# Performance work log

Measured on AMD Instinct MI355X. Metric: run time of the kernel, lower is better.

Reference implementation:

```python
import jax, jax.numpy as jnp
import numpy as np

B, L, H, G, NH, DH, FF = 16, 512, 1024, 2, 16, 64, 4096
DM = H // G          # per-group d_model = 512
LG = L // G          # inner attention seq len = 256
EPS = 1e-6


def _ln(x, g, b):
    m = x.mean(-1, keepdims=True)
    v = ((x - m) ** 2).mean(-1, keepdims=True)
    return (x - m) * jax.lax.rsqrt(v + EPS) * g + b


def setup_inputs() -> dict:
    key = jax.random.key(0)
    ks = jax.random.split(key, 12)
    sd = 0.02
    n = lambda k, sh: jax.random.normal(k, sh, jnp.float32) * sd
    return {
        "y": jax.random.normal(ks[0], (B, L, H), jnp.float32),
        "y_mask": jax.random.randint(ks[1], (B, 1, 1, LG), 0, 2).astype(bool),
        # MHAtt projections (operate on per-group d_model = DM)
        "Wv": n(ks[2], (DM, DM)), "bv": jnp.zeros((DM,), jnp.float32),
        "Wk": n(ks[3], (DM, DM)), "bk": jnp.zeros((DM,), jnp.float32),
        "Wq": n(ks[4], (DM, DM)), "bq": jnp.zeros((DM,), jnp.float32),
        # merge projection (full hidden)
        "Wm": n(ks[5], (H, H)), "bm": jnp.zeros((H,), jnp.float32),
        # GFFN: linear1 H->FF, linear2 grouped FF/G -> H/G
        "W1": n(ks[6], (H, FF)), "b1": jnp.zeros((FF,), jnp.float32),
        "W2": n(ks[7], (FF // G, H // G)), "b2": jnp.zeros((H // G,), jnp.float32),
        # LayerNorms
        "g1": jnp.ones((H,), jnp.float32), "beta1": jnp.zeros((H,), jnp.float32),
        "g2": jnp.ones((H,), jnp.float32), "beta2": jnp.zeros((H,), jnp.float32),
    }


def reference(y, y_mask, Wv, bv, Wk, bk, Wq, bq, Wm, bm, W1, b1, W2, b2,
              g1, beta1, g2, beta2):
    b, l, d = y.shape
    # group reshuffle: split channels into G groups, stack along batch
    yg = jnp.concatenate(jnp.split(y, G, axis=-1), axis=0)        # (b*G, l, DM)
    mask = jnp.tile(y_mask, (G, 1, 1, 1))                          # (b*G, 1, 1, l/G)

    # projections; view uses h*dh = H so inner seq becomes l/G
    q = (yg @ Wq + bq).reshape(b * G, -1, NH, DH).transpose(0, 2, 1, 3)  # (bG, NH, l/G, DH)
    k = (yg @ Wk + bk).reshape(b * G, -1, NH, DH).transpose(0, 2, 1, 3)
    v = (yg @ Wv + bv).reshape(b * G, -1, NH, DH).transpose(0, 2, 1, 3)

    scores = jnp.einsum('bhqd,bhkd->bhqk', q, k) / np.sqrt(DH)
    scores = jnp.where(mask, jnp.float32(-1e9), scores)
    att = jax.nn.softmax(scores, axis=-1)                          # dropout = identity (eval)
    ctx = jnp.einsum('bhqk,bhkd->bhqd', att, v)                    # (bG, NH, l/G, DH)
    ctx = ctx.transpose(0, 2, 1, 3).reshape(b * G, -1, DM)         # (bG, l, DM)

    atted = jnp.concatenate(jnp.split(ctx, G, axis=0), axis=-1)    # (b, l, H)
    atted = atted @ Wm + bm
    y1 = _ln(y + atted, g1, beta1)

    # GFFN
    h1 = jax.nn.relu(y1 @ W1 + b1)                                  # (b, l, FF)
    h2 = jnp.einsum('blgf,fo->blgo', h1.reshape(b, l, G, FF // G), W2) + b2
    ff = h2.reshape(b, l, H)
    return _ln(y1 + ff, g2, beta2)
```

## Files before the change

### kernel.cpp

```cpp
#include <hip/hip_runtime.h>
#include <stdint.h>

typedef unsigned short u16;
using us8   = __attribute__((ext_vector_type(8))) unsigned short;
using us4   = __attribute__((ext_vector_type(4))) unsigned short;
using bf16x8 = __attribute__((ext_vector_type(8))) __bf16;
using f32x4 = __attribute__((ext_vector_type(4))) float;

#define DEV static __device__ __forceinline__

DEV float bf2f(u16 u) { union { uint32_t i; float f; } v; v.i = (uint32_t)u << 16; return v.f; }
DEV u16 f2bf(float f) {
    union { float f; uint32_t i; } v; v.f = f;
    uint32_t u = v.i;
    return (u16)((u + 0x7FFFu + ((u >> 16) & 1u)) >> 16);
}

DEV void async16(const u16* g, u16* ldsbase)
{
    __builtin_amdgcn_global_load_lds((const __attribute__((address_space(1))) void*)g,
                                     (__attribute__((address_space(3))) void*)ldsbase, 16, 0, 0);
}

struct DetectArgs { const void* p[18]; int nw[18]; };

__global__ __launch_bounds__(256) void k_detect_all(DetectArgs a, int* flags)
{
    const int b = blockIdx.x;
    const int t = threadIdx.x;
    __shared__ int cnt[4];
    if (t < 4) cnt[t] = 0;
    __syncthreads();
    if (b == 1) {
        const uint8_t* m = (const uint8_t*)a.p[1];
        int c0 = 0, c1 = 0, c2 = 0, c3 = 0;
        for (int i = t; i < 4096; i += 256) {
            uint8_t v = m[i];
            int mod = i & 3;
            if (v == 0x3F && mod == 1) c0++;
            if (v == 0x3F && mod == 3) c1++;
            if (v == 1 && mod != 0) c2++;
            if (v == 1 && mod == 0) c3++;
        }
        atomicAdd(&cnt[0], c0); atomicAdd(&cnt[1], c1); atomicAdd(&cnt[2], c2); atomicAdd(&cnt[3], c3);
        __syncthreads();
        if (t == 0) {
            int mf;
            if (cnt[0] > 0) mf = 2;
            else if (cnt[1] > 0) mf = 3;
            else if (cnt[2] > 0) mf = 0;
            else if (cnt[3] > 0) mf = 1;
            else mf = 0;
            flags[1] = mf;
        }
    } else {
        const u16* p = (const u16*)a.p[b];
        int nw = a.nw[b];
        int nze = 0, pe = 0, nzo = 0;
        for (int i = t; i < nw; i += 256) {
            u16 w = p[i];
            if (w == 0) continue;
            int e = (w >> 7) & 0xFF;
            bool pl = (e >= 90 && e <= 140);
            if ((i & 1) == 0) { nze++; if (pl) pe++; }
            else nzo++;
        }
        atomicAdd(&cnt[0], nze); atomicAdd(&cnt[1], pe); atomicAdd(&cnt[2], nzo);
        __syncthreads();
        if (t == 0) {
            int f;
            if (cnt[0] > 0)      f = (cnt[1] * 10 >= cnt[0] * 6) ? 2 : 3;
            else if (cnt[2] > 0) f = 3;
            else                 f = 2;
            flags[b] = f;
        }
    }
}

__global__ __launch_bounds__(256) void k_expand_mask(const void* mask, const int* flag, float* mb)
{
    int i = blockIdx.x * 256 + threadIdx.x;
    if (i >= 4096) return;
    int f = *flag;
    bool on;
    if (f == 0)      on = ((const uint8_t*)mask)[i]  != 0;
    else if (f == 1) on = ((const int*)mask)[i]      != 0;
    else if (f == 2) on = ((const u16*)mask)[i]      != 0;
    else             on = ((const uint32_t*)mask)[i] != 0;
    mb[i] = on ? -1e9f : 0.0f;
}

__global__ __launch_bounds__(256) void k_convert_bf(const void* src, u16* dst, int n, const int* flag)
{
    int i = blockIdx.x * 256 + threadIdx.x;
    if (i >= n) return;
    if (*flag == 2) dst[i] = ((const u16*)src)[i];
    else            dst[i] = f2bf(((const float*)src)[i]);
}

struct TransArgs { const void* src[6]; u16* dst[6]; int R[6]; int C[6]; int flagidx[6]; int tstart[7]; };

__global__ __launch_bounds__(256) void k_transpose_all(TransArgs a, const int* flags)
{
    const int tb = blockIdx.x;
    int s = 0;
    while (tb >= a.tstart[s + 1]) s++;
    const int lt = tb - a.tstart[s];
    const int R = a.R[s], C = a.C[s];
    const int tilesX = C >> 5;
    const int ti = lt / tilesX, tj = lt - ti * tilesX;
    const int r0 = ti * 32, c0 = tj * 32;
    const bool isbf = (flags[a.flagidx[s]] == 2);
    const int t = threadIdx.x;
    const int j = t & 31, i0 = t >> 5;
    __shared__ u16 tile[32][33];
#pragma unroll
    for (int p = 0; p < 4; p++) {
        int r = r0 + i0 + p * 8;
        size_t idx = (size_t)r * C + c0 + j;
        u16 v = isbf ? ((const u16*)a.src[s])[idx] : f2bf(((const float*)a.src[s])[idx]);
        tile[i0 + p * 8][j] = v;
    }
    __syncthreads();
    u16* dst = a.dst[s];
#pragma unroll
    for (int p = 0; p < 4; p++) {
        int c = i0 + p * 8;
        dst[(size_t)(c0 + c) * R + r0 + j] = tile[j][c];
    }
}

struct ConvArgs { const void* src[10]; int flagidx[10]; int off[10]; int n[10]; };

__global__ __launch_bounds__(256) void k_convert_params(ConvArgs a, const int* flags, float* par)
{
    int i = blockIdx.x * 256 + threadIdx.x;
    if (i >= 11264) return;
    int s = 0;
    while (s < 9 && i >= a.off[s] + a.n[s]) s++;
    int j = i - a.off[s];
    float v;
    if (flags[a.flagidx[s]] == 2) v = bf2f(((const u16*)a.src[s])[j]);
    else                          v = ((const float*)a.src[s])[j];
    par[i] = v;
}

template<int BM, int BN, int WR, int WC, int TM, int TN>
DEV void gemm_tile(const u16* __restrict__ A, int lda,
                   const u16* __restrict__ Bt, int ldb, int K,
                   u16* As, u16* Bs, f32x4 (&acc)[TM][TN])
{
    const int t = threadIdx.x;
    const int lane = t & 63;
    const int wave = t >> 6;
    const int wr = wave / WC;
    const int wc = wave % WC;
    const int m16 = lane & 15;
    const int quad = lane >> 4;
    const int lr8 = lane >> 3;
    const int lsw = (((lane & 7) ^ lr8) << 3);

#pragma unroll
    for (int i = 0; i < TM; i++)
#pragma unroll
        for (int j = 0; j < TN; j++) {
            acc[i][j][0] = 0.f; acc[i][j][1] = 0.f; acc[i][j][2] = 0.f; acc[i][j][3] = 0.f;
        }

    for (int kb = 0; kb < K; kb += 64) {
#pragma unroll
        for (int i = 0; i < BM / 32; i++) {
            int chunk = wave * (BM / 32) + i;
            int r = chunk * 8 + lr8;
            async16(A + (size_t)r * lda + kb + lsw, As + chunk * 512);
        }
#pragma unroll
        for (int i = 0; i < BN / 32; i++) {
            int chunk = wave * (BN / 32) + i;
            int r = chunk * 8 + lr8;
            async16(Bt + (size_t)r * ldb + kb + lsw, Bs + chunk * 512);
        }
        __syncthreads();
#pragma unroll
        for (int ks = 0; ks < 2; ks++) {
            bf16x8 af[TM], bfr[TN];
#pragma unroll
            for (int i = 0; i < TM; i++) {
                int row = wr * TM * 16 + i * 16 + m16;
                int jq = ks * 4 + quad;
                af[i] = *(const bf16x8*)(As + row * 64 + ((jq ^ (row & 7)) << 3));
            }
#pragma unroll
            for (int j = 0; j < TN; j++) {
                int row = wc * TN * 16 + j * 16 + m16;
                int jq = ks * 4 + quad;
                bfr[j] = *(const bf16x8*)(Bs + row * 64 + ((jq ^ (row & 7)) << 3));
            }
#pragma unroll
            for (int i = 0; i < TM; i++)
#pragma unroll
                for (int j = 0; j < TN; j++)
                    acc[i][j] = __builtin_amdgcn_mfma_f32_16x16x32_bf16(af[i], bfr[j], acc[i][j], 0, 0, 0);
        }
        __syncthreads();
    }
}

template<bool RELU>
__global__ __launch_bounds__(256) void k_gemm_std(const u16* __restrict__ A, int lda,
                                                  const u16* __restrict__ Bt, int ldb,
                                                  const float* __restrict__ bias,
                                                  u16* __restrict__ C, int ldc, int K)
{
    __shared__ __align__(16) u16 As[128 * 64];
    __shared__ __align__(16) u16 Bs[128 * 64];
    const u16* Ab = A + (size_t)blockIdx.y * 128 * lda;
    const u16* Bb = Bt + (size_t)blockIdx.x * 128 * ldb;
    f32x4 acc[4][4];
    gemm_tile<128, 128, 2, 2, 4, 4>(Ab, lda, Bb, ldb, K, As, Bs, acc);

    const int t = threadIdx.x, lane = t & 63, wave = t >> 6;
    const int wr = wave >> 1, wc = wave & 1, m16 = lane & 15, quad = lane >> 4;
    const size_t rowBase = (size_t)blockIdx.y * 128 + wr * 64;
    const int colBase = blockIdx.x * 128 + wc * 64;
#pragma unroll
    for (int tm = 0; tm < 4; tm++)
#pragma unroll
        for (int tn = 0; tn < 4; tn++) {
            int col = colBase + tn * 16 + m16;
            float bv = bias ? bias[col] : 0.f;
#pragma unroll
            for (int r = 0; r < 4; r++) {
                size_t row = rowBase + tm * 16 + quad * 4 + r;
                float v = acc[tm][tn][r] + bv;
                if (RELU) v = fmaxf(v, 0.f);
                C[row * (size_t)ldc + col] = f2bf(v);
            }
        }
}

__global__ __launch_bounds__(256) void k_gemm_qkv(const u16* __restrict__ y_c,
                                                  const u16* __restrict__ WqT,
                                                  const u16* __restrict__ WkT,
                                                  const u16* __restrict__ WvT,
                                                  const float* __restrict__ biases,
                                                  u16* __restrict__ qp, u16* __restrict__ kp, u16* __restrict__ vp)
{
    __shared__ __align__(16) u16 As[128 * 64];
    __shared__ __align__(16) u16 Bs[128 * 64];
    const int z = blockIdx.z;
    const int mat = z % 3, g = z / 3;
    const u16* Bt = (mat == 0) ? WqT : (mat == 1) ? WkT : WvT;
    u16* out = ((mat == 0) ? qp : (mat == 1) ? kp : vp) + (size_t)g * 4194304;
    const float* bias = biases + mat * 512;
    const u16* Ab = y_c + g * 512 + (size_t)blockIdx.y * 128 * 1024;
    const u16* Bb = Bt + (size_t)blockIdx.x * 128 * 512;
    f32x4 acc[4][4];
    gemm_tile<128, 128, 2, 2, 4, 4>(Ab, 1024, Bb, 512, 512, As, Bs, acc);

    const int t = threadIdx.x, lane = t & 63, wave = t >> 6;
    const int wr = wave >> 1, wc = wave & 1, m16 = lane & 15, quad = lane >> 4;
    const size_t rowBase = (size_t)blockIdx.y * 128 + wr * 64;
    const int colBase = blockIdx.x * 128 + wc * 64;
#pragma unroll
    for (int tm = 0; tm < 4; tm++)
#pragma unroll
        for (int tn = 0; tn < 4; tn++) {
            int col = colBase + tn * 16 + m16;
            float bv = bias[col];
#pragma unroll
            for (int r = 0; r < 4; r++) {
                size_t row = rowBase + tm * 16 + quad * 4 + r;
                out[row * 512 + col] = f2bf(acc[tm][tn][r] + bv);
            }
        }
}

__global__ __launch_bounds__(256) void k_transpose_v(const u16* __restrict__ vproj, u16* __restrict__ vT)
{
    __shared__ __align__(16) u16 tile[64 * 72];
    const int lt = blockIdx.x, hlow = blockIdx.y, bg = blockIdx.z;
    const int t = threadIdx.x;
    {
        int rl = t >> 2, c16 = (t & 3) * 16;
        const u16* src = vproj + (size_t)bg * 262144 + (size_t)(lt * 64 + rl) * 512 + hlow * 64 + c16;
        *(us8*)(tile + rl * 72 + c16)     = *(const us8*)src;
        *(us8*)(tile + rl * 72 + c16 + 8) = *(const us8*)(src + 8);
    }
    __syncthreads();
    const int lanej = t & 31, grp = t >> 5;
#pragma unroll
    for (int hbit = 0; hbit < 2; hbit++) {
        int h = hbit * 8 + hlow;
#pragma unroll
        for (int i = 0; i < 8; i++) {
            int dh = grp + i * 8;
            u16 val = tile[(2 * lanej + hbit) * 72 + dh];
            vT[(((size_t)bg * 16 + h) * 64 + dh) * 256 + lt * 32 + lanej] = val;
        }
    }
}

__global__ __launch_bounds__(512, 2) void k_attn_fused(const u16* __restrict__ qproj,
                                                       const u16* __restrict__ kproj,
                                                       const u16* __restrict__ vT,
                                                       const float* __restrict__ maskb,
                                                       u16* __restrict__ attedpre)
{
    __shared__ __align__(16) u16 Ks[256 * 64];
    __shared__ __align__(16) u16 Vs[64 * 256];
    __shared__ __align__(16) u16 Ps[8 * 2 * 2048];

    const int z = blockIdx.x;
    const int bg = z >> 4, h = z & 15, hbit = h >> 3, hlow = h & 7;
    const int b = bg & 15, g = bg >> 4;
    const int t = threadIdx.x, lane = t & 63, wave = t >> 6;
    const int m16 = lane & 15, quad = lane >> 4;
    const int lr8 = lane >> 3;
    const int lsw = (((lane & 7) ^ lr8) << 3);

    const size_t base = (size_t)bg * 262144 + (size_t)hbit * 512 + (size_t)hlow * 64;
    const u16* Qb = qproj + base;
    const u16* Kb = kproj + base;

#pragma unroll
    for (int i = 0; i < 4; i++) {
        int chunk = wave * 4 + i;
        int row = chunk * 8 + lr8;
        async16(Kb + (size_t)row * 1024 + lsw, Ks + chunk * 512);
    }
    const u16* Vb = vT + (size_t)z * 16384;
#pragma unroll
    for (int i = 0; i < 4; i++) {
        int chunk = wave * 4 + i;
        int d = chunk * 2 + (lane >> 5);
        int jl = lane & 31;
        int jsrc = (jl & 24) | ((jl & 7) ^ (d & 7));
        async16(Vb + (size_t)d * 256 + jsrc * 8, Vs + chunk * 512);
    }

    bf16x8 qf[2][2];
#pragma unroll
    for (int mt = 0; mt < 2; mt++)
#pragma unroll
        for (int ks = 0; ks < 2; ks++) {
            int qrow = wave * 32 + mt * 16 + m16;
            qf[mt][ks] = *(const bf16x8*)(Qb + (size_t)qrow * 1024 + ks * 32 + quad * 8);
        }
    float mb[16];
#pragma unroll
    for (int nt = 0; nt < 16; nt++) mb[nt] = maskb[b * 256 + nt * 16 + m16];

    __syncthreads();

    f32x4 s[2][16];
#pragma unroll
    for (int mt = 0; mt < 2; mt++)
#pragma unroll
        for (int nt = 0; nt < 16; nt++) { s[mt][nt][0] = 0.f; s[mt][nt][1] = 0.f; s[mt][nt][2] = 0.f; s[mt][nt][3] = 0.f; }
#pragma unroll
    for (int ks = 0; ks < 2; ks++) {
        int jq = ks * 4 + quad;
#pragma unroll
        for (int nt = 0; nt < 16; nt++) {
            int row = nt * 16 + m16;
            bf16x8 kf = *(const bf16x8*)(Ks + row * 64 + ((jq ^ (row & 7)) << 3));
#pragma unroll
            for (int mt = 0; mt < 2; mt++)
                s[mt][nt] = __builtin_amdgcn_mfma_f32_16x16x32_bf16(qf[mt][ks], kf, s[mt][nt], 0, 0, 0);
        }
    }

    float rinv[2][4];
#pragma unroll
    for (int mt = 0; mt < 2; mt++)
#pragma unroll
        for (int r = 0; r < 4; r++) {
            float mm = -3.0e38f;
#pragma unroll
            for (int nt = 0; nt < 16; nt++) {
                float v = s[mt][nt][r] * 0.125f + mb[nt];
                s[mt][nt][r] = v;
                mm = fmaxf(mm, v);
            }
            mm = fmaxf(mm, __shfl_xor(mm, 1));
            mm = fmaxf(mm, __shfl_xor(mm, 2));
            mm = fmaxf(mm, __shfl_xor(mm, 4));
            mm = fmaxf(mm, __shfl_xor(mm, 8));
            float ss = 0.f;
#pragma unroll
            for (int nt = 0; nt < 16; nt++) {
                float e = __expf(s[mt][nt][r] - mm);
                s[mt][nt][r] = e;
                ss += e;
            }
            ss += __shfl_xor(ss, 1);
            ss += __shfl_xor(ss, 2);
            ss += __shfl_xor(ss, 4);
            ss += __shfl_xor(ss, 8);
            rinv[mt][r] = 1.0f / ss;
        }

    f32x4 ctx[2][4];
#pragma unroll
    for (int mt = 0; mt < 2; mt++)
#pragma unroll
        for (int dt = 0; dt < 4; dt++) { ctx[mt][dt][0] = 0.f; ctx[mt][dt][1] = 0.f; ctx[mt][dt][2] = 0.f; ctx[mt][dt][3] = 0.f; }

#pragma unroll
    for (int kc = 0; kc < 4; kc++) {
        u16* Pb = Ps + wave * 4096 + (kc & 1) * 2048;
#pragma unroll
        for (int mt = 0; mt < 2; mt++)
#pragma unroll
            for (int nl = 0; nl < 4; nl++) {
                int nt = kc * 4 + nl;
#pragma unroll
                for (int r = 0; r < 4; r++) {
                    int row = mt * 16 + quad * 4 + r;
                    int col = nl * 16 + m16;
                    int j = col >> 3, e = col & 7;
                    Pb[row * 64 + (((j ^ (row & 7)) << 3) | e)] = f2bf(s[mt][nt][r] * rinv[mt][r]);
                }
            }
#pragma unroll
        for (int ks = 0; ks < 2; ks++) {
            int jq = ks * 4 + quad;
            bf16x8 pf[2];
#pragma unroll
            for (int mt = 0; mt < 2; mt++) {
                int row = mt * 16 + m16;
                pf[mt] = *(const bf16x8*)(Pb + row * 64 + ((jq ^ (row & 7)) << 3));
            }
#pragma unroll
            for (int dt = 0; dt < 4; dt++) {
                int d = dt * 16 + m16;
                int j = kc * 8 + ks * 4 + quad;
                int slot = (j & 24) | ((j & 7) ^ (d & 7));
                bf16x8 vf = *(const bf16x8*)(Vs + d * 256 + slot * 8);
#pragma unroll
                for (int mt = 0; mt < 2; mt++)
                    ctx[mt][dt] = __builtin_amdgcn_mfma_f32_16x16x32_bf16(pf[mt], vf, ctx[mt][dt], 0, 0, 0);
            }
        }
    }

    const int cBase = g * 512 + hlow * 64;
#pragma unroll
    for (int mt = 0; mt < 2; mt++)
#pragma unroll
        for (int dt = 0; dt < 4; dt++) {
            int dh = dt * 16 + m16;
#pragma unroll
            for (int r = 0; r < 4; r++) {
                int sI = wave * 32 + mt * 16 + quad * 4 + r;
                int l = 2 * sI + hbit;
                attedpre[((size_t)b * 512 + l) * 1024 + cBase + dh] = f2bf(ctx[mt][dt][r]);
            }
        }
}

__global__ __launch_bounds__(256) void k_gemm_ffn2(const u16* __restrict__ h1,
                                                   const u16* __restrict__ W2T,
                                                   const float* __restrict__ b2,
                                                   u16* __restrict__ out)
{
    __shared__ __align__(16) u16 As[128 * 64];
    __shared__ __align__(16) u16 Bs[128 * 64];
    const int xi = blockIdx.x;
    const int g = xi >> 2, xn = xi & 3;
    const u16* Ab = h1 + (size_t)blockIdx.y * 128 * 4096 + g * 2048;
    const u16* Bb = W2T + (size_t)xn * 128 * 2048;
    f32x4 acc[4][4];
    gemm_tile<128, 128, 2, 2, 4, 4>(Ab, 4096, Bb, 2048, 2048, As, Bs, acc);

    const int t = threadIdx.x, lane = t & 63, wave = t >> 6;
    const int wr = wave >> 1, wc = wave & 1, m16 = lane & 15, quad = lane >> 4;
    const size_t rowBase = (size_t)blockIdx.y * 128 + wr * 64;
    const int colg = xn * 128 + wc * 64;
#pragma unroll
    for (int tm = 0; tm < 4; tm++)
#pragma unroll
        for (int tn = 0; tn < 4; tn++) {
            int cg = colg + tn * 16 + m16;
            float bv = b2[cg];
#pragma unroll
            for (int r = 0; r < 4; r++) {
                size_t row = rowBase + tm * 16 + quad * 4 + r;
                out[row * 1024 + g * 512 + cg] = f2bf(acc[tm][tn][r] + bv);
            }
        }
}

template<int FINAL>
__global__ __launch_bounds__(256) void k_ln(const u16* __restrict__ x1, const u16* __restrict__ x2,
                                            const float* __restrict__ gamma, const float* __restrict__ beta,
                                            void* __restrict__ outv, const int* __restrict__ yflag)
{
    const size_t row = blockIdx.x;
    const int t = threadIdx.x;
    us4 a = *(const us4*)(x1 + row * 1024 + t * 4);
    us4 b = *(const us4*)(x2 + row * 1024 + t * 4);
    float v[4]; float s = 0.f, s2 = 0.f;
#pragma unroll
    for (int i = 0; i < 4; i++) { v[i] = bf2f(a[i]) + bf2f(b[i]); s += v[i]; s2 += v[i] * v[i]; }
#pragma unroll
    for (int off = 32; off > 0; off >>= 1) { s += __shfl_xor(s, off); s2 += __shfl_xor(s2, off); }
    __shared__ float red[8];
    const int lane = t & 63, wave = t >> 6;
    if (lane == 0) { red[wave] = s; red[wave + 4] = s2; }
    __syncthreads();
    s = red[0] + red[1] + red[2] + red[3];
    s2 = red[4] + red[5] + red[6] + red[7];
    float mean = s * (1.0f / 1024.0f);
    float var = fmaxf(s2 * (1.0f / 1024.0f) - mean * mean, 0.0f);
    float rs = rsqrtf(var + 1e-6f);
    float o[4];
#pragma unroll
    for (int i = 0; i < 4; i++) {
        int c = t * 4 + i;
        o[i] = (v[i] - mean) * rs * gamma[c] + beta[c];
    }
    bool f32out = FINAL && yflag && (*yflag == 3);
    if (f32out) {
        float* out = (float*)outv;
#pragma unroll
        for (int i = 0; i < 4; i++) out[row * 1024 + t * 4 + i] = o[i];
    } else {
        u16* out = (u16*)outv;
        us4 ov;
#pragma unroll
        for (int i = 0; i < 4; i++) ov[i] = f2bf(o[i]);
        *(us4*)(out + row * 1024 + t * 4) = ov;
    }
}

extern "C" void kernel_launch(void* const* d_in, const int* in_sizes, int n_in,
                              void* d_out, int out_size, void* d_ws, size_t ws_size,
                              hipStream_t stream)
{
    (void)in_sizes; (void)n_in; (void)out_size; (void)ws_size;
    const void* y    = d_in[0];
    const void* mask = d_in[1];
    const void* Wv = d_in[2];  const void* bv = d_in[3];
    const void* Wk = d_in[4];  const void* bk = d_in[5];
    const void* Wq = d_in[6];  const void* bq = d_in[7];
    const void* Wm = d_in[8];  const void* bm = d_in[9];
    const void* W1 = d_in[10]; const void* b1 = d_in[11];
    const void* W2 = d_in[12]; const void* b2 = d_in[13];
    const void* g1 = d_in[14]; const void* be1 = d_in[15];
    const void* g2 = d_in[16]; const void* be2 = d_in[17];

    char* ws = (char*)d_ws;
    size_t off = 0;
    auto alloc = [&](size_t bytes) { void* p = ws + off; off = (off + bytes + 255) & ~(size_t)255; return p; };

    int*   flags = (int*)alloc(32 * 4);
    float* maskb = (float*)alloc(16 * 256 * 4);
    float* par   = (float*)alloc(11264 * 4);
    u16* WqT  = (u16*)alloc((size_t)262144 * 2);
    u16* WkT  = (u16*)alloc((size_t)262144 * 2);
    u16* WvT  = (u16*)alloc((size_t)262144 * 2);
    u16* WmT  = (u16*)alloc((size_t)1048576 * 2);
    u16* W1T  = (u16*)alloc((size_t)4194304 * 2);
    u16* W2T  = (u16*)alloc((size_t)1048576 * 2);
    u16* y_c  = (u16*)alloc((size_t)8388608 * 2);
    u16* slotA = (u16*)alloc((size_t)8388608 * 2);
    u16* slotB = (u16*)alloc((size_t)8388608 * 2);
    u16* slotC = (u16*)alloc((size_t)8388608 * 2);
    u16* slotD = (u16*)alloc((size_t)8388608 * 2);
    u16* Pbig  = (u16*)alloc((size_t)33554432 * 2);

    float* p_bm  = par + 1536;
    float* p_b1  = par + 2560;
    float* p_b2  = par + 6656;
    float* p_g1  = par + 7168;
    float* p_be1 = par + 8192;
    float* p_g2  = par + 9216;
    float* p_be2 = par + 10240;

    DetectArgs da;
    {
        const void* srcs[18] = {y, mask, Wv, bv, Wk, bk, Wq, bq, Wm, bm, W1, b1, W2, b2, g1, be1, g2, be2};
        const int   nele[18] = {8388608, 4096, 262144, 512, 262144, 512, 262144, 512, 1048576, 1024,
                                4194304, 4096, 1048576, 512, 1024, 1024, 1024, 1024};
        for (int i = 0; i < 18; i++) { da.p[i] = srcs[i]; da.nw[i] = nele[i] < 4096 ? nele[i] : 4096; }
    }
    k_detect_all<<<18, 256, 0, stream>>>(da, flags);

    k_expand_mask<<<16, 256, 0, stream>>>(mask, flags + 1, maskb);
    k_convert_bf<<<32768, 256, 0, stream>>>(y, y_c, 8388608, flags + 0);

    TransArgs ta;
    {
        const void* s6[6] = {Wq, Wk, Wv, Wm, W1, W2};
        u16* d6[6] = {WqT, WkT, WvT, WmT, W1T, W2T};
        int R6[6] = {512, 512, 512, 1024, 1024, 2048};
        int C6[6] = {512, 512, 512, 1024, 4096, 512};
        int f6[6] = {6, 4, 2, 8, 10, 12};
        int ts[7] = {0, 256, 512, 768, 1792, 5888, 6912};
        for (int i = 0; i < 6; i++) { ta.src[i] = s6[i]; ta.dst[i] = d6[i]; ta.R[i] = R6[i]; ta.C[i] = C6[i]; ta.flagidx[i] = f6[i]; }
        for (int i = 0; i < 7; i++) ta.tstart[i] = ts[i];
    }
    k_transpose_all<<<6912, 256, 0, stream>>>(ta, flags);

    ConvArgs ca;
    {
        const void* s10[10] = {bq, bk, bv, bm, b1, b2, g1, be1, g2, be2};
        int f10[10] = {7, 5, 3, 9, 11, 13, 14, 15, 16, 17};
        int o10[10] = {0, 512, 1024, 1536, 2560, 6656, 7168, 8192, 9216, 10240};
        int n10[10] = {512, 512, 512, 1024, 4096, 512, 1024, 1024, 1024, 1024};
        for (int i = 0; i < 10; i++) { ca.src[i] = s10[i]; ca.flagidx[i] = f10[i]; ca.off[i] = o10[i]; ca.n[i] = n10[i]; }
    }
    k_convert_params<<<44, 256, 0, stream>>>(ca, flags, par);

    u16* qproj = slotA;
    u16* kproj = slotB;
    u16* vT    = slotC;
    u16* vproj = slotD;

    k_gemm_qkv<<<dim3(4, 64, 6), 256, 0, stream>>>(y_c, WqT, WkT, WvT, par, qproj, kproj, vproj);
    k_transpose_v<<<dim3(8, 8, 32), 256, 0, stream>>>(vproj, vT);

    u16* attedpre = slotD;
    k_attn_fused<<<512, 512, 0, stream>>>(qproj, kproj, vT, maskb, attedpre);

    u16* mergeout = slotA;
    k_gemm_std<false><<<dim3(8, 64), 256, 0, stream>>>(attedpre, 1024, WmT, 1024, p_bm, mergeout, 1024, 1024);

    u16* y1 = slotB;
    k_ln<0><<<8192, 256, 0, stream>>>(y_c, mergeout, p_g1, p_be1, y1, nullptr);

    u16* h1 = Pbig;
    k_gemm_std<true><<<dim3(32, 64), 256, 0, stream>>>(y1, 1024, W1T, 1024, p_b1, h1, 4096, 1024);

    u16* ffout = slotC;
    k_gemm_ffn2<<<dim3(8, 64), 256, 0, stream>>>(h1, W2T, p_b2, ffout);

    k_ln<1><<<8192, 256, 0, stream>>>(y1, ffout, p_g2, p_be2, d_out, flags + 0);
}
```

Measured before the change: 423.8 us.

## Fuse QKV projection and V transpose into the attention kernel

```diff
diff --git a/kernel.cpp b/kernel.cpp
--- a/kernel.cpp
+++ b/kernel.cpp
@@ -239,77 +239,22 @@
         }
 }
 
-__global__ __launch_bounds__(256) void k_gemm_qkv(const u16* __restrict__ y_c,
-                                                  const u16* __restrict__ WqT,
-                                                  const u16* __restrict__ WkT,
-                                                  const u16* __restrict__ WvT,
-                                                  const float* __restrict__ biases,
-                                                  u16* __restrict__ qp, u16* __restrict__ kp, u16* __restrict__ vp)
-{
-    __shared__ __align__(16) u16 As[128 * 64];
-    __shared__ __align__(16) u16 Bs[128 * 64];
-    const int z = blockIdx.z;
-    const int mat = z % 3, g = z / 3;
-    const u16* Bt = (mat == 0) ? WqT : (mat == 1) ? WkT : WvT;
-    u16* out = ((mat == 0) ? qp : (mat == 1) ? kp : vp) + (size_t)g * 4194304;
-    const float* bias = biases + mat * 512;
-    const u16* Ab = y_c + g * 512 + (size_t)blockIdx.y * 128 * 1024;
-    const u16* Bb = Bt + (size_t)blockIdx.x * 128 * 512;
-    f32x4 acc[4][4];
-    gemm_tile<128, 128, 2, 2, 4, 4>(Ab, 1024, Bb, 512, 512, As, Bs, acc);
-
-    const int t = threadIdx.x, lane = t & 63, wave = t >> 6;
-    const int wr = wave >> 1, wc = wave & 1, m16 = lane & 15, quad = lane >> 4;
-    const size_t rowBase = (size_t)blockIdx.y * 128 + wr * 64;
-    const int colBase = blockIdx.x * 128 + wc * 64;
-#pragma unroll
-    for (int tm = 0; tm < 4; tm++)
-#pragma unroll
-        for (int tn = 0; tn < 4; tn++) {
-            int col = colBase + tn * 16 + m16;
-            float bv = bias[col];
-#pragma unroll
-            for (int r = 0; r < 4; r++) {
-                size_t row = rowBase + tm * 16 + quad * 4 + r;
-                out[row * 512 + col] = f2bf(acc[tm][tn][r] + bv);
-            }
-        }
-}
-
-__global__ __launch_bounds__(256) void k_transpose_v(const u16* __restrict__ vproj, u16* __restrict__ vT)
-{
-    __shared__ __align__(16) u16 tile[64 * 72];
-    const int lt = blockIdx.x, hlow = blockIdx.y, bg = blockIdx.z;
-    const int t = threadIdx.x;
-    {
-        int rl = t >> 2, c16 = (t & 3) * 16;
-        const u16* src = vproj + (size_t)bg * 262144 + (size_t)(lt * 64 + rl) * 512 + hlow * 64 + c16;
-        *(us8*)(tile + rl * 72 + c16)     = *(const us8*)src;
-        *(us8*)(tile + rl * 72 + c16 + 8) = *(const us8*)(src + 8);
-    }
-    __syncthreads();
-    const int lanej = t & 31, grp = t >> 5;
-#pragma unroll
-    for (int hbit = 0; hbit < 2; hbit++) {
-        int h = hbit * 8 + hlow;
-#pragma unroll
-        for (int i = 0; i < 8; i++) {
-            int dh = grp + i * 8;
-            u16 val = tile[(2 * lanej + hbit) * 72 + dh];
-            vT[(((size_t)bg * 16 + h) * 64 + dh) * 256 + lt * 32 + lanej] = val;
-        }
-    }
-}
-
-__global__ __launch_bounds__(512, 2) void k_attn_fused(const u16* __restrict__ qproj,
-                                                       const u16* __restrict__ kproj,
-                                                       const u16* __restrict__ vT,
-                                                       const float* __restrict__ maskb,
-                                                       u16* __restrict__ attedpre)
-{
-    __shared__ __align__(16) u16 Ks[256 * 64];
-    __shared__ __align__(16) u16 Vs[64 * 256];
-    __shared__ __align__(16) u16 Ps[8 * 2 * 2048];
+__global__ __launch_bounds__(512, 2) void k_qkv_attn(const u16* __restrict__ y_c,
+                                                     const u16* __restrict__ WqT,
+                                                     const u16* __restrict__ WkT,
+                                                     const u16* __restrict__ WvT,
+                                                     const float* __restrict__ par,
+                                                     const float* __restrict__ maskb,
+                                                     u16* __restrict__ attedpre)
+{
+    __shared__ __align__(16) u16 smem[49152];
+    u16* As  = smem;
+    u16* Wqs = smem + 16384;
+    u16* Wks = smem + 20480;
+    u16* Wvs = smem + 24576;
+    u16* Ks  = smem;
+    u16* Vs  = smem + 16384;
+    u16* Pw8 = smem + 32768;
 
     const int z = blockIdx.x;
     const int bg = z >> 4, h = z & 15, hbit = h >> 3, hlow = h & 7;
@@ -319,33 +264,94 @@
     const int lr8 = lane >> 3;
     const int lsw = (((lane & 7) ^ lr8) << 3);
 
-    const size_t base = (size_t)bg * 262144 + (size_t)hbit * 512 + (size_t)hlow * 64;
-    const u16* Qb = qproj + base;
-    const u16* Kb = kproj + base;
-
-#pragma unroll
-    for (int i = 0; i < 4; i++) {
-        int chunk = wave * 4 + i;
-        int row = chunk * 8 + lr8;
-        async16(Kb + (size_t)row * 1024 + lsw, Ks + chunk * 512);
-    }
-    const u16* Vb = vT + (size_t)z * 16384;
-#pragma unroll
-    for (int i = 0; i < 4; i++) {
-        int chunk = wave * 4 + i;
-        int d = chunk * 2 + (lane >> 5);
-        int jl = lane & 31;
-        int jsrc = (jl & 24) | ((jl & 7) ^ (d & 7));
-        async16(Vb + (size_t)d * 256 + jsrc * 8, Vs + chunk * 512);
-    }
-
+    const u16* Yb = y_c + (size_t)(b * 512 + hbit) * 1024 + g * 512;
+
+    f32x4 aq[2][4], ak[2][4], av[2][4];
+#pragma unroll
+    for (int i = 0; i < 2; i++)
+#pragma unroll
+        for (int j = 0; j < 4; j++) {
+            aq[i][j][0]=0.f; aq[i][j][1]=0.f; aq[i][j][2]=0.f; aq[i][j][3]=0.f;
+            ak[i][j][0]=0.f; ak[i][j][1]=0.f; ak[i][j][2]=0.f; ak[i][j][3]=0.f;
+            av[i][j][0]=0.f; av[i][j][1]=0.f; av[i][j][2]=0.f; av[i][j][3]=0.f;
+        }
+
+    for (int c = 0; c < 8; ++c) {
+        const int kb = c * 64;
+#pragma unroll
+        for (int i = 0; i < 4; i++) {
+            int chunk = wave * 4 + i;
+            int srow = chunk * 8 + lr8;
+            async16(Yb + (size_t)srow * 2048 + kb + lsw, As + chunk * 512);
+        }
+        {
+            int row = wave * 8 + lr8;
+            const size_t woff = (size_t)(hlow * 64 + row) * 512 + kb + lsw;
+            async16(WqT + woff, Wqs + wave * 512);
+            async16(WkT + woff, Wks + wave * 512);
+            async16(WvT + woff, Wvs + wave * 512);
+        }
+        __syncthreads();
+#pragma unroll
+        for (int ks = 0; ks < 2; ks++) {
+            const int jq = ks * 4 + quad;
+            bf16x8 af[2];
+#pragma unroll
+            for (int mt = 0; mt < 2; mt++) {
+                int row = wave * 32 + mt * 16 + m16;
+                af[mt] = *(const bf16x8*)(As + row * 64 + ((jq ^ (row & 7)) << 3));
+            }
+#pragma unroll
+            for (int tn = 0; tn < 4; tn++) {
+                int rowb = tn * 16 + m16;
+                int offb = rowb * 64 + ((jq ^ (rowb & 7)) << 3);
+                bf16x8 wq = *(const bf16x8*)(Wqs + offb);
+                bf16x8 wk = *(const bf16x8*)(Wks + offb);
+                bf16x8 wv = *(const bf16x8*)(Wvs + offb);
+#pragma unroll
+                for (int mt = 0; mt < 2; mt++) {
+                    aq[mt][tn] = __builtin_amdgcn_mfma_f32_16x16x32_bf16(af[mt], wq, aq[mt][tn], 0, 0, 0);
+                    ak[mt][tn] = __builtin_amdgcn_mfma_f32_16x16x32_bf16(af[mt], wk, ak[mt][tn], 0, 0, 0);
+                    av[mt][tn] = __builtin_amdgcn_mfma_f32_16x16x32_bf16(af[mt], wv, av[mt][tn], 0, 0, 0);
+                }
+            }
+        }
+        __syncthreads();
+    }
+
+    float bQ[4], bK[4], bV[4];
+#pragma unroll
+    for (int tn = 0; tn < 4; tn++) {
+        int c0 = hlow * 64 + tn * 16 + m16;
+        bQ[tn] = par[c0]; bK[tn] = par[512 + c0]; bV[tn] = par[1024 + c0];
+    }
+    u16* Qw = Pw8 + wave * 2048;
+#pragma unroll
+    for (int tm = 0; tm < 2; tm++)
+#pragma unroll
+        for (int tn = 0; tn < 4; tn++) {
+            int dh = tn * 16 + m16;
+#pragma unroll
+            for (int r = 0; r < 4; r++) {
+                int sl = tm * 16 + quad * 4 + r;
+                int s_ = wave * 32 + sl;
+                Ks[s_ * 64 + ((((dh >> 3) ^ (s_ & 7)) << 3) | (dh & 7))] = f2bf(ak[tm][tn][r] + bK[tn]);
+                {
+                    int j = s_ >> 3;
+                    int slot = (j & 24) | ((j & 7) ^ (dh & 7));
+                    Vs[dh * 256 + slot * 8 + (s_ & 7)] = f2bf(av[tm][tn][r] + bV[tn]);
+                }
+                Qw[sl * 64 + ((((dh >> 3) ^ (sl & 7)) << 3) | (dh & 7))] = f2bf(aq[tm][tn][r] + bQ[tn]);
+            }
+        }
     bf16x8 qf[2][2];
 #pragma unroll
     for (int mt = 0; mt < 2; mt++)
 #pragma unroll
         for (int ks = 0; ks < 2; ks++) {
-            int qrow = wave * 32 + mt * 16 + m16;
-            qf[mt][ks] = *(const bf16x8*)(Qb + (size_t)qrow * 1024 + ks * 32 + quad * 8);
+            int row = mt * 16 + m16;
+            int jq = ks * 4 + quad;
+            qf[mt][ks] = *(const bf16x8*)(Qw + row * 64 + ((jq ^ (row & 7)) << 3));
         }
     float mb[16];
 #pragma unroll
@@ -357,7 +363,7 @@
 #pragma unroll
     for (int mt = 0; mt < 2; mt++)
 #pragma unroll
-        for (int nt = 0; nt < 16; nt++) { s[mt][nt][0] = 0.f; s[mt][nt][1] = 0.f; s[mt][nt][2] = 0.f; s[mt][nt][3] = 0.f; }
+        for (int nt = 0; nt < 16; nt++) { s[mt][nt][0]=0.f; s[mt][nt][1]=0.f; s[mt][nt][2]=0.f; s[mt][nt][3]=0.f; }
 #pragma unroll
     for (int ks = 0; ks < 2; ks++) {
         int jq = ks * 4 + quad;
@@ -405,11 +411,10 @@
 #pragma unroll
     for (int mt = 0; mt < 2; mt++)
 #pragma unroll
-        for (int dt = 0; dt < 4; dt++) { ctx[mt][dt][0] = 0.f; ctx[mt][dt][1] = 0.f; ctx[mt][dt][2] = 0.f; ctx[mt][dt][3] = 0.f; }
+        for (int dt = 0; dt < 4; dt++) { ctx[mt][dt][0]=0.f; ctx[mt][dt][1]=0.f; ctx[mt][dt][2]=0.f; ctx[mt][dt][3]=0.f; }
 
 #pragma unroll
     for (int kc = 0; kc < 4; kc++) {
-        u16* Pb = Ps + wave * 4096 + (kc & 1) * 2048;
 #pragma unroll
         for (int mt = 0; mt < 2; mt++)
 #pragma unroll
@@ -420,7 +425,7 @@
                     int row = mt * 16 + quad * 4 + r;
                     int col = nl * 16 + m16;
                     int j = col >> 3, e = col & 7;
-                    Pb[row * 64 + (((j ^ (row & 7)) << 3) | e)] = f2bf(s[mt][nt][r] * rinv[mt][r]);
+                    Qw[row * 64 + (((j ^ (row & 7)) << 3) | e)] = f2bf(s[mt][nt][r] * rinv[mt][r]);
                 }
             }
 #pragma unroll
@@ -430,7 +435,7 @@
 #pragma unroll
             for (int mt = 0; mt < 2; mt++) {
                 int row = mt * 16 + m16;
-                pf[mt] = *(const bf16x8*)(Pb + row * 64 + ((jq ^ (row & 7)) << 3));
+                pf[mt] = *(const bf16x8*)(Qw + row * 64 + ((jq ^ (row & 7)) << 3));
             }
 #pragma unroll
             for (int dt = 0; dt < 4; dt++) {
@@ -614,16 +619,8 @@
     }
     k_convert_params<<<44, 256, 0, stream>>>(ca, flags, par);
 
-    u16* qproj = slotA;
-    u16* kproj = slotB;
-    u16* vT    = slotC;
-    u16* vproj = slotD;
-
-    k_gemm_qkv<<<dim3(4, 64, 6), 256, 0, stream>>>(y_c, WqT, WkT, WvT, par, qproj, kproj, vproj);
-    k_transpose_v<<<dim3(8, 8, 32), 256, 0, stream>>>(vproj, vT);
-
     u16* attedpre = slotD;
-    k_attn_fused<<<512, 512, 0, stream>>>(qproj, kproj, vT, maskb, attedpre);
+    k_qkv_attn<<<512, 512, 0, stream>>>(y_c, WqT, WkT, WvT, par, maskb, attedpre);
 
     u16* mergeout = slotA;
     k_gemm_std<false><<<dim3(8, 64), 256, 0, stream>>>(attedpre, 1024, WmT, 1024, p_bm, mergeout, 1024, 1024);
```

Result: faster. 415.4 us (-2.0%).
